# Performance work log

Hardware: AMD Instinct MI355X
Metric: run time of the kernel (lower is better)

The kernel has to match this reference:

```python
import jax, jax.numpy as jnp
import numpy as np

B, T, D, L, H = 8, 2048, 128, 4, 2
HD = D // H
NITEMS = 200000
EPS = 1e-8  # RMSNorm eps and HSTU denom eps


def _rms(x, s):
    return x * jax.lax.rsqrt(jnp.mean(x * x, axis=-1, keepdims=True) + EPS) * s


def setup_inputs() -> dict:
    key = jax.random.key(0)
    ks = jax.random.split(key, 16)
    g = lambda k, shape: jax.random.normal(k, shape, jnp.float32) * 0.02
    inp = {}
    inp["log_seqs"] = jax.random.randint(ks[0], (B, T), 1, NITEMS + 1)
    inp["attn_mask"] = jnp.tril(jnp.ones((T, T), dtype=bool))  # causal keep-mask
    inp["item_table"] = g(ks[1], (NITEMS + 1, D))
    inp["pos_table"] = g(ks[2], (2 * T + 1, D))
    inp["emb_ln_s"] = jnp.ones((D,), jnp.float32)
    inp["ln1_s"] = jnp.ones((L, D), jnp.float32)
    inp["Uw"] = g(ks[3], (L, D, D)); inp["Ub"] = jnp.zeros((L, D), jnp.float32)
    inp["Vw"] = g(ks[4], (L, D, D)); inp["Vb"] = jnp.zeros((L, D), jnp.float32)
    inp["Qw"] = g(ks[5], (L, D, D)); inp["Qb"] = jnp.zeros((L, D), jnp.float32)
    inp["Kw"] = g(ks[6], (L, D, D)); inp["Kb"] = jnp.zeros((L, D), jnp.float32)
    inp["f2w"] = g(ks[7], (L, D, D)); inp["f2b"] = jnp.zeros((L, D), jnp.float32)
    inp["hstu_ln_s"] = jnp.ones((L, D), jnp.float32)
    inp["ln2_s"] = jnp.ones((L, D), jnp.float32)
    inp["c1w"] = g(ks[8], (L, D, D)); inp["c1b"] = jnp.zeros((L, D), jnp.float32)
    inp["c2w"] = g(ks[9], (L, D, D)); inp["c2b"] = jnp.zeros((L, D), jnp.float32)
    inp["last_ln_s"] = jnp.ones((D,), jnp.float32)
    return inp


def reference(log_seqs, attn_mask, item_table, pos_table, emb_ln_s, ln1_s,
              Uw, Ub, Vw, Vb, Qw, Qb, Kw, Kb, f2w, f2b, hstu_ln_s, ln2_s,
              c1w, c1b, c2w, c2b, last_ln_s):
    positions = jnp.arange(1, T + 1)
    x = item_table[log_seqs] + pos_table[positions][None]  # (B,T,D)
    x = _rms(x, emb_ln_s)
    keep = attn_mask[None, None]  # (1,1,T,T) broadcast over (B,H,T,T)
    scale = 1.0 / np.sqrt(HD)
    for i in range(L):
        q = _rms(x, ln1_s[i])  # pre-norm (norm_first)
        U = jax.nn.silu(q @ Uw[i] + Ub[i])
        V = jax.nn.silu(q @ Vw[i] + Vb[i])
        Q = jax.nn.silu(q @ Qw[i] + Qb[i])
        K = jax.nn.silu(q @ Kw[i] + Kb[i])
        Qh = Q.reshape(B, T, H, HD)
        Kh = K.reshape(B, T, H, HD)
        Vh = V.reshape(B, T, H, HD)
        logits = jnp.einsum('bthd,bshd->bhts', Qh, Kh) * scale  # (B,H,T,T)
        A = jnp.maximum(jax.nn.silu(logits), 0.0)  # SiLU then clamp_min(0)
        A = jnp.where(keep, A, 0.0)
        denom = jnp.sum(A, axis=-1, keepdims=True)
        A = jnp.where(denom > 1e-12, A / (denom + EPS), 0.0)
        AV = jnp.einsum('bhts,bshd->bthd', A, Vh).reshape(B, T, D)
        y = (_rms(AV, hstu_ln_s[i]) * U) @ f2w[i] + f2b[i]
        x = x + y
        f = _rms(x, ln2_s[i])  # pre-norm for FFN
        h = jax.nn.gelu(f @ c1w[i] + c1b[i], approximate=False)  # Conv1d k=1 == Linear
        x = x + (h @ c2w[i] + c2b[i])
    return _rms(x, last_ln_s)
```

## Files before the change

### kernel.cpp

```cpp
#include <hip/hip_runtime.h>
#include <hip/hip_bf16.h>

typedef __bf16 bf16x8 __attribute__((ext_vector_type(8)));
typedef float f32x4 __attribute__((ext_vector_type(4)));
using bf16 = __hip_bfloat16;

constexpr int T = 2048;
constexpr int M = 8 * 2048;

__device__ inline float ldf(const void* p, size_t i, int isf32) {
  if (isf32) return ((const float*)p)[i];
  unsigned u = ((const unsigned short*)p)[i];
  return __uint_as_float(u << 16);
}
__device__ inline float bf2f(unsigned short u) { return __uint_as_float((unsigned)u << 16); }
__device__ inline unsigned short bfb(float x) {
  __hip_bfloat16 h = __float2bfloat16(x);
  return *reinterpret_cast<unsigned short*>(&h);
}

struct PPtrs { const void* p[12]; };

__global__ void detect_convert_k(const void* __restrict__ item, PPtrs ps,
                                 float* __restrict__ params, int* __restrict__ flagp) {
  __shared__ int cnt[4];
  __shared__ int flagLDS;
  int tid = threadIdx.x;
  unsigned short lo = ((const unsigned short*)item)[tid * 2];
  float a = fabsf(bf2f(lo));
  bool okb = (a > 1e-5f) && (a < 0.5f);
  unsigned long long m = __ballot(okb);
  if ((tid & 63) == 0) cnt[tid >> 6] = __popcll(m);
  __syncthreads();
  if (tid == 0) {
    int tot = cnt[0] + cnt[1] + cnt[2] + cnt[3];
    int f = (tot < 128) ? 1 : 0;
    flagLDS = f; *flagp = f;
  }
  __syncthreads();
  int f = flagLDS;
  const int lens[12] = {128, 512, 512, 512, 128, 512, 512, 512, 512, 512, 512, 512};
  int off = 0;
  for (int j = 0; j < 12; ++j) {
    for (int i = tid; i < lens[j]; i += 256) params[off + i] = ldf(ps.p[j], i, f);
    off += lens[j];
  }
}

struct WPtrs { const void* p[7]; };

__global__ void transpose_w_k(WPtrs w, bf16* __restrict__ dst, const int* __restrict__ flagp) {
  int f = *flagp;
  int l = blockIdx.x, wi = blockIdx.y;
  const void* s = w.p[wi];
  size_t sbase = (size_t)l * 16384;
  bf16* d = dst + ((size_t)wi * 4 + l) * 16384;
  for (int i = 0; i < 64; ++i) {
    int e = i * 256 + threadIdx.x;
    d[e] = __float2bfloat16(ldf(s, sbase + (size_t)(e & 127) * 128 + (e >> 7), f));
  }
}

__device__ inline void issueW(const bf16* wt, bf16x8 (&w)[4][8], int quad, int l16) {
  #pragma unroll
  for (int kk = 0; kk < 4; ++kk)
    #pragma unroll
    for (int nt = 0; nt < 8; ++nt)
      w[kk][nt] = *(const bf16x8*)(wt + (size_t)(nt * 16 + l16) * 128 + kk * 32 + quad * 8);
}
__device__ inline void mfma_stage(const bf16x8 (&a)[4], const bf16x8 (&w)[4][8], f32x4 (&acc)[8]) {
  #pragma unroll
  for (int kk = 0; kk < 4; ++kk)
    #pragma unroll
    for (int nt = 0; nt < 8; ++nt)
      acc[nt] = __builtin_amdgcn_mfma_f32_16x16x32_bf16(a[kk], w[kk][nt], acc[nt], 0, 0, 0);
}
__device__ inline void zero8(f32x4 (&acc)[8]) {
  #pragma unroll
  for (int i = 0; i < 8; ++i) acc[i] = (f32x4){0.f, 0.f, 0.f, 0.f};
}
__device__ inline void readA(const bf16* aw, bf16x8 (&a)[4], int quad, int l16) {
  #pragma unroll
  for (int kk = 0; kk < 4; ++kk)
    a[kk] = *(const bf16x8*)&aw[l16 * 136 + kk * 32 + quad * 8];
}
__device__ inline void buildA_rms(const float (&xr)[8][4], const float* scale, bf16* aw,
                                  int quad, int l16) {
  float s8[8];
  #pragma unroll
  for (int nt = 0; nt < 8; ++nt) s8[nt] = scale[nt * 16 + l16];
  #pragma unroll
  for (int r = 0; r < 4; ++r) {
    float ss = 0.f;
    #pragma unroll
    for (int nt = 0; nt < 8; ++nt) ss += xr[nt][r] * xr[nt][r];
    ss += __shfl_xor(ss, 1); ss += __shfl_xor(ss, 2);
    ss += __shfl_xor(ss, 4); ss += __shfl_xor(ss, 8);
    float rs = rsqrtf(ss * (1.f / 128.f) + 1e-8f);
    #pragma unroll
    for (int nt = 0; nt < 8; ++nt)
      aw[(quad * 4 + r) * 136 + nt * 16 + l16] = __float2bfloat16(xr[nt][r] * rs * s8[nt]);
  }
}
__device__ inline void epi_silu_store(const f32x4 (&acc)[8], const float* bias, bf16* outg,
                                      int row0, int quad, int l16, float mulf) {
  #pragma unroll
  for (int nt = 0; nt < 8; ++nt) {
    int col = nt * 16 + l16; float bv = bias[col];
    #pragma unroll
    for (int r = 0; r < 4; ++r) {
      float v = acc[nt][r] + bv;
      v = v / (1.f + __expf(-v)) * mulf;
      outg[(size_t)(row0 + quad * 4 + r) * 128 + col] = __float2bfloat16(v);
    }
  }
}
__device__ inline void epi_silu_vt(const f32x4 (&acc)[8], const float* bias, bf16* vtg,
                                   int row0, int quad, int l16) {
  #pragma unroll
  for (int nt = 0; nt < 8; ++nt) {
    int col = nt * 16 + l16; float bv = bias[col];
    int h = col >> 6, hd = col & 63;
    #pragma unroll
    for (int r = 0; r < 4; ++r) {
      int gr = row0 + quad * 4 + r; int b = gr >> 11, t = gr & 2047;
      float v = acc[nt][r] + bv; v = v / (1.f + __expf(-v));
      vtg[((size_t)(b * 2 + h) * 64 + hd) * 2048 + t] = __float2bfloat16(v);
    }
  }
}
__device__ inline void epi_addx(const f32x4 (&acc)[8], const float* bias, float (&xr)[8][4],
                                int l16) {
  #pragma unroll
  for (int nt = 0; nt < 8; ++nt) {
    float bv = bias[nt * 16 + l16];
    #pragma unroll
    for (int r = 0; r < 4; ++r) xr[nt][r] += acc[nt][r] + bv;
  }
}

__device__ inline void qkvu_stages(const float (&xr)[8][4], bf16* aw, const bf16* wT,
    const float* params, int lnext, bf16* Ug, bf16* Qg, bf16* Kg, bf16* VTg,
    int row0, int quad, int l16) {
  buildA_rms(xr, params + 128 + lnext * 128, aw, quad, l16);
  bf16x8 a[4]; readA(aw, a, quad, l16);
  bf16x8 w[4][8]; f32x4 acc[8];
  const float* pb = params + 1792;
  issueW(wT + (size_t)(0 * 4 + lnext) * 16384, w, quad, l16);
  zero8(acc); mfma_stage(a, w, acc);
  issueW(wT + (size_t)(1 * 4 + lnext) * 16384, w, quad, l16);
  epi_silu_store(acc, pb + 0 * 512 + lnext * 128, Ug, row0, quad, l16, 1.f);
  zero8(acc); mfma_stage(a, w, acc);
  issueW(wT + (size_t)(2 * 4 + lnext) * 16384, w, quad, l16);
  epi_silu_vt(acc, pb + 1 * 512 + lnext * 128, VTg, row0, quad, l16);
  zero8(acc); mfma_stage(a, w, acc);
  issueW(wT + (size_t)(3 * 4 + lnext) * 16384, w, quad, l16);
  epi_silu_store(acc, pb + 2 * 512 + lnext * 128, Qg, row0, quad, l16, 0.125f);
  zero8(acc); mfma_stage(a, w, acc);
  epi_silu_store(acc, pb + 3 * 512 + lnext * 128, Kg, row0, quad, l16, 1.f);
}

__global__ __launch_bounds__(256) void pre_k(const int* __restrict__ seqs,
    const void* __restrict__ item, const void* __restrict__ pos, const bf16* __restrict__ wT,
    const float* __restrict__ params, float* __restrict__ xg, bf16* __restrict__ Ug,
    bf16* __restrict__ Qg, bf16* __restrict__ Kg, bf16* __restrict__ VTg,
    const int* __restrict__ flagp) {
  __shared__ __align__(16) bf16 awAll[4][16 * 136 + 8];
  int f = *flagp;
  int tid = threadIdx.x, wv = tid >> 6, lane = tid & 63, quad = lane >> 4, l16 = lane & 15;
  bf16* aw = awAll[wv];
  int row0 = blockIdx.x * 64 + wv * 16;
  int idxs[4];
  #pragma unroll
  for (int r = 0; r < 4; ++r) idxs[r] = seqs[row0 + quad * 4 + r];
  float xr[8][4];
  #pragma unroll
  for (int nt = 0; nt < 8; ++nt) {
    int col = nt * 16 + l16;
    #pragma unroll
    for (int r = 0; r < 4; ++r) {
      int gr = row0 + quad * 4 + r; int t = gr & 2047;
      xr[nt][r] = ldf(item, (size_t)idxs[r] * 128 + col, f)
                + ldf(pos, (size_t)(t + 1) * 128 + col, f);
    }
  }
  {
    float s8[8];
    #pragma unroll
    for (int nt = 0; nt < 8; ++nt) s8[nt] = params[nt * 16 + l16];
    #pragma unroll
    for (int r = 0; r < 4; ++r) {
      float ss = 0.f;
      #pragma unroll
      for (int nt = 0; nt < 8; ++nt) ss += xr[nt][r] * xr[nt][r];
      ss += __shfl_xor(ss, 1); ss += __shfl_xor(ss, 2);
      ss += __shfl_xor(ss, 4); ss += __shfl_xor(ss, 8);
      float rs = rsqrtf(ss * (1.f / 128.f) + 1e-8f);
      #pragma unroll
      for (int nt = 0; nt < 8; ++nt) xr[nt][r] *= rs * s8[nt];
    }
  }
  #pragma unroll
  for (int nt = 0; nt < 8; ++nt)
    #pragma unroll
    for (int r = 0; r < 4; ++r)
      xg[(size_t)(row0 + quad * 4 + r) * 128 + nt * 16 + l16] = xr[nt][r];
  qkvu_stages(xr, aw, wT, params, 0, Ug, Qg, Kg, VTg, row0, quad, l16);
}

__global__ __launch_bounds__(256) void post_k(int l, float* __restrict__ xg,
    const float* __restrict__ avg, bf16* __restrict__ Ug, bf16* __restrict__ Qg,
    bf16* __restrict__ Kg, bf16* __restrict__ VTg, const bf16* __restrict__ wT,
    const float* __restrict__ params, void* __restrict__ dout, const int* __restrict__ flagp) {
  __shared__ __align__(16) bf16 awAll[4][16 * 136 + 8];
  int tid = threadIdx.x, wv = tid >> 6, lane = tid & 63, quad = lane >> 4, l16 = lane & 15;
  bf16* aw = awAll[wv];
  int row0 = blockIdx.x * 64 + wv * 16;
  bf16x8 w[4][8]; f32x4 acc[8];
  issueW(wT + (size_t)(16 + l) * 16384, w, quad, l16);
  float xr[8][4], av[8][4], uu[8][4];
  #pragma unroll
  for (int nt = 0; nt < 8; ++nt) {
    int col = nt * 16 + l16;
    #pragma unroll
    for (int r = 0; r < 4; ++r) {
      size_t off = (size_t)(row0 + quad * 4 + r) * 128 + col;
      xr[nt][r] = xg[off];
      av[nt][r] = avg[off];
      uu[nt][r] = bf2f(((const unsigned short*)Ug)[off]);
    }
  }
  {
    const float* hs = params + 640 + l * 128;
    float s8[8];
    #pragma unroll
    for (int nt = 0; nt < 8; ++nt) s8[nt] = hs[nt * 16 + l16];
    #pragma unroll
    for (int r = 0; r < 4; ++r) {
      float ss = 0.f;
      #pragma unroll
      for (int nt = 0; nt < 8; ++nt) ss += av[nt][r] * av[nt][r];
      ss += __shfl_xor(ss, 1); ss += __shfl_xor(ss, 2);
      ss += __shfl_xor(ss, 4); ss += __shfl_xor(ss, 8);
      float rs = rsqrtf(ss * (1.f / 128.f) + 1e-8f);
      #pragma unroll
      for (int nt = 0; nt < 8; ++nt)
        aw[(quad * 4 + r) * 136 + nt * 16 + l16] =
            __float2bfloat16(av[nt][r] * rs * s8[nt] * uu[nt][r]);
    }
  }
  bf16x8 a[4]; readA(aw, a, quad, l16);
  zero8(acc); mfma_stage(a, w, acc);
  issueW(wT + (size_t)(20 + l) * 16384, w, quad, l16);
  epi_addx(acc, params + 3840 + l * 128, xr, l16);
  buildA_rms(xr, params + 1152 + l * 128, aw, quad, l16);
  readA(aw, a, quad, l16);
  zero8(acc); mfma_stage(a, w, acc);
  issueW(wT + (size_t)(24 + l) * 16384, w, quad, l16);
  {
    const float* bb = params + 4352 + l * 128;
    #pragma unroll
    for (int nt = 0; nt < 8; ++nt) {
      int col = nt * 16 + l16; float bv = bb[col];
      #pragma unroll
      for (int r = 0; r < 4; ++r) {
        float v = acc[nt][r] + bv;
        v = 0.5f * v * (1.f + erff(v * 0.70710678118f));
        aw[(quad * 4 + r) * 136 + col] = __float2bfloat16(v);
      }
    }
  }
  readA(aw, a, quad, l16);
  zero8(acc); mfma_stage(a, w, acc);
  epi_addx(acc, params + 4864 + l * 128, xr, l16);
  if (l == 3) {
    int f = *flagp;
    const float* ls = params + 1664;
    float s8[8];
    #pragma unroll
    for (int nt = 0; nt < 8; ++nt) s8[nt] = ls[nt * 16 + l16];
    #pragma unroll
    for (int r = 0; r < 4; ++r) {
      float ss = 0.f;
      #pragma unroll
      for (int nt = 0; nt < 8; ++nt) ss += xr[nt][r] * xr[nt][r];
      ss += __shfl_xor(ss, 1); ss += __shfl_xor(ss, 2);
      ss += __shfl_xor(ss, 4); ss += __shfl_xor(ss, 8);
      float rs = rsqrtf(ss * (1.f / 128.f) + 1e-8f);
      #pragma unroll
      for (int nt = 0; nt < 8; ++nt) {
        size_t off = (size_t)(row0 + quad * 4 + r) * 128 + nt * 16 + l16;
        float o = xr[nt][r] * rs * s8[nt];
        if (f) ((float*)dout)[off] = o; else ((unsigned short*)dout)[off] = bfb(o);
      }
    }
    return;
  }
  #pragma unroll
  for (int nt = 0; nt < 8; ++nt)
    #pragma unroll
    for (int r = 0; r < 4; ++r)
      xg[(size_t)(row0 + quad * 4 + r) * 128 + nt * 16 + l16] = xr[nt][r];
  qkvu_stages(xr, aw, wT, params, l + 1, Ug, Qg, Kg, VTg, row0, quad, l16);
}

__device__ inline void fk_loadK(const bf16* kbase, bf16x8 (&kf)[2][4], int quad, int l16) {
  #pragma unroll
  for (int kk = 0; kk < 2; ++kk)
    #pragma unroll
    for (int nt = 0; nt < 4; ++nt)
      kf[kk][nt] = *(const bf16x8*)(kbase + (size_t)(nt * 16 + l16) * 128 + kk * 32 + quad * 8);
}

__device__ inline void flash_body(int kt, int ntile, const bf16* kga, const bf16* vba,
    const bf16x8 (&qf)[2][2], const bf16x8 (&kc)[2][4], bf16x8 (&kn)[2][4],
    f32x4 (&oacc)[2][4], f32x4 (&dacc)[2], const bf16x8& onesf,
    bf16* sm, int r0, int quad, int l16) {
  int s0 = kt * 64;
  bf16x8 vf[2][4];
  #pragma unroll
  for (int kk = 0; kk < 2; ++kk)
    #pragma unroll
    for (int nt = 0; nt < 4; ++nt)
      vf[kk][nt] = *(const bf16x8*)(vba + (size_t)(nt * 16 + l16) * 2048 + s0 + kk * 32 + quad * 8);
  f32x4 sacc[2][4] = {};
  #pragma unroll
  for (int kk = 0; kk < 2; ++kk)
    #pragma unroll
    for (int nt = 0; nt < 4; ++nt) {
      sacc[0][nt] = __builtin_amdgcn_mfma_f32_16x16x32_bf16(qf[0][kk], kc[kk][nt], sacc[0][nt], 0, 0, 0);
      sacc[1][nt] = __builtin_amdgcn_mfma_f32_16x16x32_bf16(qf[1][kk], kc[kk][nt], sacc[1][nt], 0, 0, 0);
    }
  if (kt + 2 < ntile) fk_loadK(kga + (size_t)(s0 + 128) * 128, kn, quad, l16);
  #pragma unroll
  for (int mi = 0; mi < 2; ++mi) {
    int trow = r0 + mi * 16 + quad * 4;
    #pragma unroll
    for (int nt = 0; nt < 4; ++nt) {
      int sc = s0 + nt * 16 + l16;
      #pragma unroll
      for (int r = 0; r < 4; ++r) {
        float v = sacc[mi][nt][r];
        float aa = (sc <= trow + r && v > 0.f) ? v / (1.f + __expf(-v)) : 0.f;
        sm[(mi * 16 + quad * 4 + r) * 72 + nt * 16 + l16] = __float2bfloat16(aa);
      }
    }
  }
  #pragma unroll
  for (int kk = 0; kk < 2; ++kk) {
    bf16x8 af0 = *(const bf16x8*)&sm[l16 * 72 + kk * 32 + quad * 8];
    bf16x8 af1 = *(const bf16x8*)&sm[(16 + l16) * 72 + kk * 32 + quad * 8];
    #pragma unroll
    for (int nt = 0; nt < 4; ++nt) {
      oacc[0][nt] = __builtin_amdgcn_mfma_f32_16x16x32_bf16(af0, vf[kk][nt], oacc[0][nt], 0, 0, 0);
      oacc[1][nt] = __builtin_amdgcn_mfma_f32_16x16x32_bf16(af1, vf[kk][nt], oacc[1][nt], 0, 0, 0);
    }
    dacc[0] = __builtin_amdgcn_mfma_f32_16x16x32_bf16(af0, onesf, dacc[0], 0, 0, 0);
    dacc[1] = __builtin_amdgcn_mfma_f32_16x16x32_bf16(af1, onesf, dacc[1], 0, 0, 0);
  }
}

__global__ __launch_bounds__(128, 2) void flash_k(const bf16* __restrict__ Qg,
    const bf16* __restrict__ Kg, const bf16* __restrict__ VTg, float* __restrict__ avg) {
  __shared__ __align__(16) bf16 smem[2 * 2304];
  int q32 = 63 - (int)blockIdx.x;
  int bh = blockIdx.y, b = bh >> 1, h = bh & 1;
  int tid = threadIdx.x, p = tid >> 6, lane = tid & 63, quad = lane >> 4, l16 = lane & 15;
  int r0 = q32 * 32;
  bf16* sm = smem + p * 2304;
  const bf16* kga = Kg + (size_t)b * 2048 * 128 + h * 64;
  const bf16* vba = VTg + (size_t)bh * 64 * 2048;
  const bf16* qbase = Qg + ((size_t)b * 2048 + r0) * 128 + h * 64;
  bf16x8 qf[2][2];
  #pragma unroll
  for (int mi = 0; mi < 2; ++mi)
    #pragma unroll
    for (int kk = 0; kk < 2; ++kk)
      qf[mi][kk] = *(const bf16x8*)(qbase + (size_t)(mi * 16 + l16) * 128 + kk * 32 + quad * 8);
  bf16x8 onesf;
  #pragma unroll
  for (int j = 0; j < 8; ++j) onesf[j] = (l16 == 0) ? (__bf16)1.0f : (__bf16)0.0f;
  f32x4 oacc[2][4] = {};
  f32x4 dacc[2] = {};
  int ntile = q32 / 2 + 1;
  bf16x8 kA[2][4], kB[2][4];
  int kt = p;
  if (kt < ntile) {
    fk_loadK(kga + (size_t)kt * 64 * 128, kA, quad, l16);
    while (true) {
      flash_body(kt, ntile, kga, vba, qf, kA, kB, oacc, dacc, onesf, sm, r0, quad, l16);
      kt += 2;
      if (kt >= ntile) break;
      flash_body(kt, ntile, kga, vba, qf, kB, kA, oacc, dacc, onesf, sm, r0, quad, l16);
      kt += 2;
      if (kt >= ntile) break;
    }
  }
  __syncthreads();
  float* mo = (float*)smem;
  float* md = mo + 2048;
  if (p == 1) {
    #pragma unroll
    for (int mi = 0; mi < 2; ++mi) {
      #pragma unroll
      for (int nt = 0; nt < 4; ++nt)
        #pragma unroll
        for (int r = 0; r < 4; ++r)
          mo[(mi * 16 + quad * 4 + r) * 64 + nt * 16 + l16] = oacc[mi][nt][r];
      if (l16 == 0) {
        #pragma unroll
        for (int r = 0; r < 4; ++r) md[mi * 16 + quad * 4 + r] = dacc[mi][r];
      }
    }
  }
  __syncthreads();
  if (p == 0) {
    #pragma unroll
    for (int mi = 0; mi < 2; ++mi) {
      #pragma unroll
      for (int r = 0; r < 4; ++r) {
        float dn = __shfl(dacc[mi][r], quad << 4) + md[mi * 16 + quad * 4 + r];
        float inv = (dn > 1e-12f) ? 1.f / (dn + 1e-8f) : 0.f;
        int row = r0 + mi * 16 + quad * 4 + r;
        #pragma unroll
        for (int nt = 0; nt < 4; ++nt) {
          float o = (oacc[mi][nt][r] + mo[(mi * 16 + quad * 4 + r) * 64 + nt * 16 + l16]) * inv;
          avg[((size_t)b * 2048 + row) * 128 + h * 64 + nt * 16 + l16] = o;
        }
      }
    }
  }
}

extern "C" void kernel_launch(void* const* d_in, const int* in_sizes, int n_in,
                              void* d_out, int out_size, void* d_ws, size_t ws_size,
                              hipStream_t stream) {
  const int* seqs = (const int*)d_in[0];
  const void* item = d_in[2];
  const void* pos  = d_in[3];

  float* params = (float*)d_ws;
  int* flagp = (int*)((char*)d_ws + 24 * 1024);
  char* base = (char*)d_ws + 32 * 1024;
  const size_t MB = 1024 * 1024;
  float* x   = (float*)base;
  float* av  = (float*)(base + 8 * MB);
  bf16* Ug   = (bf16*)(base + 16 * MB);
  bf16* Qg   = (bf16*)(base + 20 * MB);
  bf16* Kg   = (bf16*)(base + 24 * MB);
  bf16* VTg  = (bf16*)(base + 28 * MB);
  bf16* wT   = (bf16*)(base + 32 * MB);

  PPtrs pp;
  pp.p[0] = d_in[4];  pp.p[1] = d_in[5];  pp.p[2] = d_in[16]; pp.p[3] = d_in[17];
  pp.p[4] = d_in[22]; pp.p[5] = d_in[7];  pp.p[6] = d_in[9];  pp.p[7] = d_in[11];
  pp.p[8] = d_in[13]; pp.p[9] = d_in[15]; pp.p[10] = d_in[19]; pp.p[11] = d_in[21];
  detect_convert_k<<<1, 256, 0, stream>>>(item, pp, params, flagp);

  WPtrs wp;
  wp.p[0] = d_in[6]; wp.p[1] = d_in[8]; wp.p[2] = d_in[10]; wp.p[3] = d_in[12];
  wp.p[4] = d_in[14]; wp.p[5] = d_in[18]; wp.p[6] = d_in[20];
  transpose_w_k<<<dim3(4, 7), 256, 0, stream>>>(wp, wT, flagp);

  pre_k<<<M / 64, 256, 0, stream>>>(seqs, item, pos, wT, params, x, Ug, Qg, Kg, VTg, flagp);

  for (int l = 0; l < 4; ++l) {
    flash_k<<<dim3(64, 16), 128, 0, stream>>>(Qg, Kg, VTg, av);
    post_k<<<M / 64, 256, 0, stream>>>(l, x, av, Ug, Qg, Kg, VTg, wT, params, d_out, flagp);
  }
}
```

Before: 624.2 us.

## Split flash key tiles across four waves and chunk weight loads in GEMM stages

The flash kernel now runs four waves per block instead of two. Each wave strides key tiles by four, the partial sums are reduced through LDS with vectorized float4 stores, and block-to-query assignment is rotated per head to balance causal work. The causal mask check is skipped on non-diagonal tiles. The GEMM stages load weights in half-K chunks to cut register pressure, post_k loads x later, and the weight transpose is spread over more blocks. The larger block and the extra LDS reduction may lower occupancy or add overhead on short query tiles.

```diff
diff --git a/kernel.cpp b/kernel.cpp
--- a/kernel.cpp
+++ b/kernel.cpp
@@ -51,29 +51,31 @@
 
 __global__ void transpose_w_k(WPtrs w, bf16* __restrict__ dst, const int* __restrict__ flagp) {
   int f = *flagp;
-  int l = blockIdx.x, wi = blockIdx.y;
+  int l = blockIdx.x, wi = blockIdx.y, seg = blockIdx.z;
   const void* s = w.p[wi];
   size_t sbase = (size_t)l * 16384;
   bf16* d = dst + ((size_t)wi * 4 + l) * 16384;
-  for (int i = 0; i < 64; ++i) {
-    int e = i * 256 + threadIdx.x;
+  #pragma unroll
+  for (int i = 0; i < 4; ++i) {
+    int e = seg * 1024 + i * 256 + threadIdx.x;
     d[e] = __float2bfloat16(ldf(s, sbase + (size_t)(e & 127) * 128 + (e >> 7), f));
   }
 }
 
-__device__ inline void issueW(const bf16* wt, bf16x8 (&w)[4][8], int quad, int l16) {
-  #pragma unroll
-  for (int kk = 0; kk < 4; ++kk)
+__device__ inline void loadWchunk(const bf16* wt, bf16x8 (&w)[2][8], int ch, int quad, int l16) {
+  #pragma unroll
+  for (int k2 = 0; k2 < 2; ++k2)
     #pragma unroll
     for (int nt = 0; nt < 8; ++nt)
-      w[kk][nt] = *(const bf16x8*)(wt + (size_t)(nt * 16 + l16) * 128 + kk * 32 + quad * 8);
-}
-__device__ inline void mfma_stage(const bf16x8 (&a)[4], const bf16x8 (&w)[4][8], f32x4 (&acc)[8]) {
-  #pragma unroll
-  for (int kk = 0; kk < 4; ++kk)
+      w[k2][nt] = *(const bf16x8*)(wt + (size_t)(nt * 16 + l16) * 128 + (ch * 2 + k2) * 32 + quad * 8);
+}
+__device__ inline void mfma_chunk(const bf16x8 (&a)[4], const bf16x8 (&w)[2][8],
+                                  f32x4 (&acc)[8], int ch) {
+  #pragma unroll
+  for (int k2 = 0; k2 < 2; ++k2)
     #pragma unroll
     for (int nt = 0; nt < 8; ++nt)
-      acc[nt] = __builtin_amdgcn_mfma_f32_16x16x32_bf16(a[kk], w[kk][nt], acc[nt], 0, 0, 0);
+      acc[nt] = __builtin_amdgcn_mfma_f32_16x16x32_bf16(a[ch * 2 + k2], w[k2][nt], acc[nt], 0, 0, 0);
 }
 __device__ inline void zero8(f32x4 (&acc)[8]) {
   #pragma unroll
@@ -140,24 +142,35 @@
 }
 
 __device__ inline void qkvu_stages(const float (&xr)[8][4], bf16* aw, const bf16* wT,
-    const float* params, int lnext, bf16* Ug, bf16* Qg, bf16* Kg, bf16* VTg,
+    const float* params, int ln, bf16* Ug, bf16* Qg, bf16* Kg, bf16* VTg,
     int row0, int quad, int l16) {
-  buildA_rms(xr, params + 128 + lnext * 128, aw, quad, l16);
+  buildA_rms(xr, params + 128 + ln * 128, aw, quad, l16);
   bf16x8 a[4]; readA(aw, a, quad, l16);
-  bf16x8 w[4][8]; f32x4 acc[8];
+  bf16x8 w[2][8]; f32x4 acc[8];
   const float* pb = params + 1792;
-  issueW(wT + (size_t)(0 * 4 + lnext) * 16384, w, quad, l16);
-  zero8(acc); mfma_stage(a, w, acc);
-  issueW(wT + (size_t)(1 * 4 + lnext) * 16384, w, quad, l16);
-  epi_silu_store(acc, pb + 0 * 512 + lnext * 128, Ug, row0, quad, l16, 1.f);
-  zero8(acc); mfma_stage(a, w, acc);
-  issueW(wT + (size_t)(2 * 4 + lnext) * 16384, w, quad, l16);
-  epi_silu_vt(acc, pb + 1 * 512 + lnext * 128, VTg, row0, quad, l16);
-  zero8(acc); mfma_stage(a, w, acc);
-  issueW(wT + (size_t)(3 * 4 + lnext) * 16384, w, quad, l16);
-  epi_silu_store(acc, pb + 2 * 512 + lnext * 128, Qg, row0, quad, l16, 0.125f);
-  zero8(acc); mfma_stage(a, w, acc);
-  epi_silu_store(acc, pb + 3 * 512 + lnext * 128, Kg, row0, quad, l16, 1.f);
+  const bf16* wU = wT + (size_t)(0 + ln) * 16384;
+  const bf16* wV = wT + (size_t)(4 + ln) * 16384;
+  const bf16* wQ = wT + (size_t)(8 + ln) * 16384;
+  const bf16* wK = wT + (size_t)(12 + ln) * 16384;
+  zero8(acc);
+  loadWchunk(wU, w, 0, quad, l16); mfma_chunk(a, w, acc, 0);
+  loadWchunk(wU, w, 1, quad, l16); mfma_chunk(a, w, acc, 1);
+  loadWchunk(wV, w, 0, quad, l16);
+  epi_silu_store(acc, pb + 0 * 512 + ln * 128, Ug, row0, quad, l16, 1.f);
+  zero8(acc);
+  mfma_chunk(a, w, acc, 0);
+  loadWchunk(wV, w, 1, quad, l16); mfma_chunk(a, w, acc, 1);
+  loadWchunk(wQ, w, 0, quad, l16);
+  epi_silu_vt(acc, pb + 1 * 512 + ln * 128, VTg, row0, quad, l16);
+  zero8(acc);
+  mfma_chunk(a, w, acc, 0);
+  loadWchunk(wQ, w, 1, quad, l16); mfma_chunk(a, w, acc, 1);
+  loadWchunk(wK, w, 0, quad, l16);
+  epi_silu_store(acc, pb + 2 * 512 + ln * 128, Qg, row0, quad, l16, 0.125f);
+  zero8(acc);
+  mfma_chunk(a, w, acc, 0);
+  loadWchunk(wK, w, 1, quad, l16); mfma_chunk(a, w, acc, 1);
+  epi_silu_store(acc, pb + 3 * 512 + ln * 128, Kg, row0, quad, l16, 1.f);
 }
 
 __global__ __launch_bounds__(256) void pre_k(const int* __restrict__ seqs,
@@ -216,21 +229,18 @@
   int tid = threadIdx.x, wv = tid >> 6, lane = tid & 63, quad = lane >> 4, l16 = lane & 15;
   bf16* aw = awAll[wv];
   int row0 = blockIdx.x * 64 + wv * 16;
-  bf16x8 w[4][8]; f32x4 acc[8];
-  issueW(wT + (size_t)(16 + l) * 16384, w, quad, l16);
-  float xr[8][4], av[8][4], uu[8][4];
-  #pragma unroll
-  for (int nt = 0; nt < 8; ++nt) {
-    int col = nt * 16 + l16;
-    #pragma unroll
-    for (int r = 0; r < 4; ++r) {
-      size_t off = (size_t)(row0 + quad * 4 + r) * 128 + col;
-      xr[nt][r] = xg[off];
-      av[nt][r] = avg[off];
-      uu[nt][r] = bf2f(((const unsigned short*)Ug)[off]);
-    }
-  }
   {
+    float av4[8][4], uu4[8][4];
+    #pragma unroll
+    for (int nt = 0; nt < 8; ++nt) {
+      int col = nt * 16 + l16;
+      #pragma unroll
+      for (int r = 0; r < 4; ++r) {
+        size_t off = (size_t)(row0 + quad * 4 + r) * 128 + col;
+        av4[nt][r] = avg[off];
+        uu4[nt][r] = bf2f(((const unsigned short*)Ug)[off]);
+      }
+    }
     const float* hs = params + 640 + l * 128;
     float s8[8];
     #pragma unroll
@@ -239,24 +249,38 @@
     for (int r = 0; r < 4; ++r) {
       float ss = 0.f;
       #pragma unroll
-      for (int nt = 0; nt < 8; ++nt) ss += av[nt][r] * av[nt][r];
+      for (int nt = 0; nt < 8; ++nt) ss += av4[nt][r] * av4[nt][r];
       ss += __shfl_xor(ss, 1); ss += __shfl_xor(ss, 2);
       ss += __shfl_xor(ss, 4); ss += __shfl_xor(ss, 8);
       float rs = rsqrtf(ss * (1.f / 128.f) + 1e-8f);
       #pragma unroll
       for (int nt = 0; nt < 8; ++nt)
         aw[(quad * 4 + r) * 136 + nt * 16 + l16] =
-            __float2bfloat16(av[nt][r] * rs * s8[nt] * uu[nt][r]);
+            __float2bfloat16(av4[nt][r] * rs * s8[nt] * uu4[nt][r]);
     }
   }
   bf16x8 a[4]; readA(aw, a, quad, l16);
-  zero8(acc); mfma_stage(a, w, acc);
-  issueW(wT + (size_t)(20 + l) * 16384, w, quad, l16);
+  bf16x8 w[2][8]; f32x4 acc[8];
+  const bf16* wf2 = wT + (size_t)(16 + l) * 16384;
+  const bf16* wc1 = wT + (size_t)(20 + l) * 16384;
+  const bf16* wc2 = wT + (size_t)(24 + l) * 16384;
+  float xr[8][4];
+  #pragma unroll
+  for (int nt = 0; nt < 8; ++nt)
+    #pragma unroll
+    for (int r = 0; r < 4; ++r)
+      xr[nt][r] = xg[(size_t)(row0 + quad * 4 + r) * 128 + nt * 16 + l16];
+  zero8(acc);
+  loadWchunk(wf2, w, 0, quad, l16); mfma_chunk(a, w, acc, 0);
+  loadWchunk(wf2, w, 1, quad, l16); mfma_chunk(a, w, acc, 1);
+  loadWchunk(wc1, w, 0, quad, l16);
   epi_addx(acc, params + 3840 + l * 128, xr, l16);
   buildA_rms(xr, params + 1152 + l * 128, aw, quad, l16);
   readA(aw, a, quad, l16);
-  zero8(acc); mfma_stage(a, w, acc);
-  issueW(wT + (size_t)(24 + l) * 16384, w, quad, l16);
+  zero8(acc);
+  mfma_chunk(a, w, acc, 0);
+  loadWchunk(wc1, w, 1, quad, l16); mfma_chunk(a, w, acc, 1);
+  loadWchunk(wc2, w, 0, quad, l16);
   {
     const float* bb = params + 4352 + l * 128;
     #pragma unroll
@@ -271,7 +295,9 @@
     }
   }
   readA(aw, a, quad, l16);
-  zero8(acc); mfma_stage(a, w, acc);
+  zero8(acc);
+  mfma_chunk(a, w, acc, 0);
+  loadWchunk(wc2, w, 1, quad, l16); mfma_chunk(a, w, acc, 1);
   epi_addx(acc, params + 4864 + l * 128, xr, l16);
   if (l == 3) {
     int f = *flagp;
@@ -312,7 +338,7 @@
       kf[kk][nt] = *(const bf16x8*)(kbase + (size_t)(nt * 16 + l16) * 128 + kk * 32 + quad * 8);
 }
 
-__device__ inline void flash_body(int kt, int ntile, const bf16* kga, const bf16* vba,
+__device__ inline void flash_body4(int kt, int ntile, const bf16* kga, const bf16* vba,
     const bf16x8 (&qf)[2][2], const bf16x8 (&kc)[2][4], bf16x8 (&kn)[2][4],
     f32x4 (&oacc)[2][4], f32x4 (&dacc)[2], const bf16x8& onesf,
     bf16* sm, int r0, int quad, int l16) {
@@ -331,20 +357,33 @@
       sacc[0][nt] = __builtin_amdgcn_mfma_f32_16x16x32_bf16(qf[0][kk], kc[kk][nt], sacc[0][nt], 0, 0, 0);
       sacc[1][nt] = __builtin_amdgcn_mfma_f32_16x16x32_bf16(qf[1][kk], kc[kk][nt], sacc[1][nt], 0, 0, 0);
     }
-  if (kt + 2 < ntile) fk_loadK(kga + (size_t)(s0 + 128) * 128, kn, quad, l16);
-  #pragma unroll
-  for (int mi = 0; mi < 2; ++mi) {
-    int trow = r0 + mi * 16 + quad * 4;
-    #pragma unroll
-    for (int nt = 0; nt < 4; ++nt) {
-      int sc = s0 + nt * 16 + l16;
-      #pragma unroll
-      for (int r = 0; r < 4; ++r) {
-        float v = sacc[mi][nt][r];
-        float aa = (sc <= trow + r && v > 0.f) ? v / (1.f + __expf(-v)) : 0.f;
-        sm[(mi * 16 + quad * 4 + r) * 72 + nt * 16 + l16] = __float2bfloat16(aa);
+  if (kt + 4 < ntile) fk_loadK(kga + (size_t)(s0 + 256) * 128, kn, quad, l16);
+  if (kt == ntile - 1) {
+    #pragma unroll
+    for (int mi = 0; mi < 2; ++mi) {
+      int trow = r0 + mi * 16 + quad * 4;
+      #pragma unroll
+      for (int nt = 0; nt < 4; ++nt) {
+        int sc = s0 + nt * 16 + l16;
+        #pragma unroll
+        for (int r = 0; r < 4; ++r) {
+          float v = sacc[mi][nt][r];
+          float aa = (sc <= trow + r && v > 0.f) ? v / (1.f + __expf(-v)) : 0.f;
+          sm[(mi * 16 + quad * 4 + r) * 72 + nt * 16 + l16] = __float2bfloat16(aa);
+        }
       }
     }
+  } else {
+    #pragma unroll
+    for (int mi = 0; mi < 2; ++mi)
+      #pragma unroll
+      for (int nt = 0; nt < 4; ++nt)
+        #pragma unroll
+        for (int r = 0; r < 4; ++r) {
+          float v = sacc[mi][nt][r];
+          float aa = (v > 0.f) ? v / (1.f + __expf(-v)) : 0.f;
+          sm[(mi * 16 + quad * 4 + r) * 72 + nt * 16 + l16] = __float2bfloat16(aa);
+        }
   }
   #pragma unroll
   for (int kk = 0; kk < 2; ++kk) {
@@ -360,14 +399,15 @@
   }
 }
 
-__global__ __launch_bounds__(128, 2) void flash_k(const bf16* __restrict__ Qg,
+__global__ __launch_bounds__(256, 4) void flash_k(const bf16* __restrict__ Qg,
     const bf16* __restrict__ Kg, const bf16* __restrict__ VTg, float* __restrict__ avg) {
-  __shared__ __align__(16) bf16 smem[2 * 2304];
-  int q32 = 63 - (int)blockIdx.x;
-  int bh = blockIdx.y, b = bh >> 1, h = bh & 1;
-  int tid = threadIdx.x, p = tid >> 6, lane = tid & 63, quad = lane >> 4, l16 = lane & 15;
+  __shared__ __align__(16) float lds[4 * 2080];
+  int bx = blockIdx.x, bh = blockIdx.y;
+  int q32 = (bx + bh * 20) & 63;
+  int b = bh >> 1, h = bh & 1;
+  int tid = threadIdx.x, wave = tid >> 6, lane = tid & 63, quad = lane >> 4, l16 = lane & 15;
   int r0 = q32 * 32;
-  bf16* sm = smem + p * 2304;
+  bf16* sm = (bf16*)lds + wave * 2304;
   const bf16* kga = Kg + (size_t)b * 2048 * 128 + h * 64;
   const bf16* vba = VTg + (size_t)bh * 64 * 2048;
   const bf16* qbase = Qg + ((size_t)b * 2048 + r0) * 128 + h * 64;
@@ -384,22 +424,20 @@
   f32x4 dacc[2] = {};
   int ntile = q32 / 2 + 1;
   bf16x8 kA[2][4], kB[2][4];
-  int kt = p;
+  int kt = wave;
   if (kt < ntile) {
     fk_loadK(kga + (size_t)kt * 64 * 128, kA, quad, l16);
     while (true) {
-      flash_body(kt, ntile, kga, vba, qf, kA, kB, oacc, dacc, onesf, sm, r0, quad, l16);
-      kt += 2;
-      if (kt >= ntile) break;
-      flash_body(kt, ntile, kga, vba, qf, kB, kA, oacc, dacc, onesf, sm, r0, quad, l16);
-      kt += 2;
-      if (kt >= ntile) break;
+      flash_body4(kt, ntile, kga, vba, qf, kA, kB, oacc, dacc, onesf, sm, r0, quad, l16);
+      kt += 4; if (kt >= ntile) break;
+      flash_body4(kt, ntile, kga, vba, qf, kB, kA, oacc, dacc, onesf, sm, r0, quad, l16);
+      kt += 4; if (kt >= ntile) break;
     }
   }
   __syncthreads();
-  float* mo = (float*)smem;
-  float* md = mo + 2048;
-  if (p == 1) {
+  {
+    float* mo = lds + wave * 2080;
+    float* md = mo + 2048;
     #pragma unroll
     for (int mi = 0; mi < 2; ++mi) {
       #pragma unroll
@@ -414,21 +452,25 @@
     }
   }
   __syncthreads();
-  if (p == 0) {
-    #pragma unroll
-    for (int mi = 0; mi < 2; ++mi) {
-      #pragma unroll
-      for (int r = 0; r < 4; ++r) {
-        float dn = __shfl(dacc[mi][r], quad << 4) + md[mi * 16 + quad * 4 + r];
-        float inv = (dn > 1e-12f) ? 1.f / (dn + 1e-8f) : 0.f;
-        int row = r0 + mi * 16 + quad * 4 + r;
-        #pragma unroll
-        for (int nt = 0; nt < 4; ++nt) {
-          float o = (oacc[mi][nt][r] + mo[(mi * 16 + quad * 4 + r) * 64 + nt * 16 + l16]) * inv;
-          avg[((size_t)b * 2048 + row) * 128 + h * 64 + nt * 16 + l16] = o;
-        }
-      }
-    }
+  {
+    int rr = wave * 8 + (lane >> 3);
+    int c0 = (lane & 7) * 8;
+    float dn = lds[0 * 2080 + 2048 + rr] + lds[1 * 2080 + 2048 + rr]
+             + lds[2 * 2080 + 2048 + rr] + lds[3 * 2080 + 2048 + rr];
+    float inv = (dn > 1e-12f) ? 1.f / (dn + 1e-8f) : 0.f;
+    float o[8] = {};
+    #pragma unroll
+    for (int p = 0; p < 4; ++p) {
+      float4 a0 = *(const float4*)&lds[p * 2080 + rr * 64 + c0];
+      float4 a1 = *(const float4*)&lds[p * 2080 + rr * 64 + c0 + 4];
+      o[0] += a0.x; o[1] += a0.y; o[2] += a0.z; o[3] += a0.w;
+      o[4] += a1.x; o[5] += a1.y; o[6] += a1.z; o[7] += a1.w;
+    }
+    float* dst = avg + ((size_t)b * 2048 + r0 + rr) * 128 + h * 64 + c0;
+    float4 w0, w1;
+    w0.x = o[0] * inv; w0.y = o[1] * inv; w0.z = o[2] * inv; w0.w = o[3] * inv;
+    w1.x = o[4] * inv; w1.y = o[5] * inv; w1.z = o[6] * inv; w1.w = o[7] * inv;
+    *(float4*)dst = w0; *(float4*)(dst + 4) = w1;
   }
 }
 
@@ -460,12 +502,12 @@
   WPtrs wp;
   wp.p[0] = d_in[6]; wp.p[1] = d_in[8]; wp.p[2] = d_in[10]; wp.p[3] = d_in[12];
   wp.p[4] = d_in[14]; wp.p[5] = d_in[18]; wp.p[6] = d_in[20];
-  transpose_w_k<<<dim3(4, 7), 256, 0, stream>>>(wp, wT, flagp);
+  transpose_w_k<<<dim3(4, 7, 16), 256, 0, stream>>>(wp, wT, flagp);
 
   pre_k<<<M / 64, 256, 0, stream>>>(seqs, item, pos, wT, params, x, Ug, Qg, Kg, VTg, flagp);
 
   for (int l = 0; l < 4; ++l) {
-    flash_k<<<dim3(64, 16), 128, 0, stream>>>(Qg, Kg, VTg, av);
+    flash_k<<<dim3(64, 16), 256, 0, stream>>>(Qg, Kg, VTg, av);
     post_k<<<M / 64, 256, 0, stream>>>(l, x, av, Ug, Qg, Kg, VTg, wT, params, d_out, flagp);
   }
 }
```

Result: slower. 923.5 us (+48.0%).
